# Kernel optimization log

Measured on AMD Instinct MI355X. Metric: run time of the kernel, lower is better.

Reference implementation:

```python
import jax, jax.numpy as jnp
import numpy as np

D = 256        # embedding dim
H = 256        # deriv MLP hidden dim
R = 8          # number of derivation rules
V = 64         # number of thax (axiom) classes
S = 8          # number of sine levels
N_INIT = 8192  # initial clauses
L = 16         # DAG layers
M = 4096       # deriv nodes per layer
N_TOTAL = N_INIT + L * M
POS_WEIGHT_EXTRA = 1.0


def setup_inputs() -> dict:
    key = jax.random.key(0)
    ks = jax.random.split(key, 20)
    inp = {}
    # prob_tweaks (Tweak) is constant-initialized to 0.0 in the original
    inp["prob_tweaks"] = jnp.zeros((4, 2), jnp.float32)
    inp["init_table"] = jax.random.normal(ks[0], (V, D)) * 0.1
    inp["sine_table"] = jax.random.normal(ks[1], (S, D)) * 0.1
    # fan-in scaled so 16 stacked MLP layers stay numerically sane
    inp["W1"] = jax.random.normal(ks[2], (R, 2 * D, H)) / np.float32(np.sqrt(2 * D))
    inp["b1"] = jax.random.normal(ks[3], (R, H)) * 0.01
    inp["t1"] = jax.random.normal(ks[4], (R, H)) * 0.01
    inp["W2"] = jax.random.normal(ks[5], (R, H, D)) / np.float32(np.sqrt(H))
    inp["b2"] = jax.random.normal(ks[6], (R, D)) * 0.01
    inp["w_eval"] = jax.random.normal(ks[7], (D,)) / np.float32(np.sqrt(D))
    inp["b_eval"] = jax.random.normal(ks[8], (1,)) * 0.01
    inp["t_eval"] = jax.random.normal(ks[9], (1,)) * 0.01
    inp["pos"] = jax.random.uniform(ks[10], (N_TOTAL,))
    inp["neg"] = jax.random.uniform(ks[11], (N_TOTAL,))
    inp["init_thax"] = jax.random.randint(ks[12], (N_INIT,), 0, V)
    inp["init_sine"] = jax.random.randint(ks[13], (N_INIT,), 0, S)
    inp["deriv_rule"] = jax.random.randint(ks[14], (L, M), 0, R)
    # parents of layer l must point at already-computed nodes (topological order)
    pk = jax.random.split(ks[15], L)
    pars = [jax.random.randint(pk[l], (M, 2), 0, N_INIT + l * M) for l in range(L)]
    inp["deriv_parents"] = jnp.stack(pars)
    inp["labeled"] = jax.random.randint(ks[16], (N_TOTAL,), 0, 2)
    return inp


def reference(prob_tweaks, init_table, sine_table, W1, b1, t1, W2, b2,
              w_eval, b_eval, t_eval, pos, neg,
              init_thax, init_sine, deriv_rule, deriv_parents, labeled):
    tw_eval = prob_tweaks[0, 0]   # my_tweak[0] for eval_net
    tw_deriv = prob_tweaks[0, 1]  # my_tweak[1] for deriv MLPs

    # init embeddings: per-thax embedding + sine embellishment (USE_SINE)
    emb0 = init_table[init_thax] + sine_table[init_sine]       # [N_INIT, D]
    store = jnp.zeros((N_TOTAL, D), init_table.dtype).at[:N_INIT].set(emb0)

    # layered DAG walk: gather parents, apply rule-specific 2-layer MLP
    for l in range(L):
        x = store[deriv_parents[l]].reshape(M, 2 * D)          # gather parents
        oh = jax.nn.one_hot(deriv_rule[l], R, dtype=x.dtype)   # [M, R] rule dispatch
        h = jax.nn.relu(jnp.einsum('mi,rih->mrh', x, W1)
                        + b1[None] + tw_deriv * t1[None])      # [M, R, H]
        y = jnp.einsum('mrh,rhd->mrd', h, W2) + b2[None]       # [M, R, D]
        emb = jnp.einsum('mrd,mr->md', y, oh)                  # select per-node rule
        store = store.at[N_INIT + l * M:N_INIT + (l + 1) * M].set(emb)

    # eval_net: logit per node with scalar tweak
    vals = store @ w_eval + b_eval[0] + tw_eval * t_eval[0]    # [N_TOTAL]

    lab = labeled.astype(vals.dtype)
    tot = pos + neg
    target = pos / jnp.maximum(tot, 1e-8)
    tot_pos = jnp.sum(pos * lab)
    tot_neg = jnp.sum(neg * lab)
    pw = POS_WEIGHT_EXTRA * tot_neg / jnp.maximum(tot_pos, 1e-8)

    # BCEWithLogitsLoss(pos_weight=pw), contribution weighted by (pos+neg)
    ls = jax.nn.log_sigmoid(vals)
    lns = jax.nn.log_sigmoid(-vals)
    bce = -(pw * target * ls + (1.0 - target) * lns)
    loss = jnp.sum(lab * tot * bce).reshape(1)

    posOK = jnp.sum(lab * pos * (vals >= 0.0))
    negOK = jnp.sum(lab * neg * (vals < 0.0))
    return (loss, posOK, negOK, tot_pos, tot_neg)
```

## Files before the change

kernel.cpp:

```cpp
#include <hip/hip_runtime.h>
#include <math.h>

#define D_    256
#define H_    256
#define R_    8
#define NINIT 8192
#define LL    16
#define MM    4096
#define NTOT  (NINIT + LL*MM)
#define TB    16
#define MP    (MM + R_*TB)
#define NB    (MP/TB)
#define KS1   16
#define KS2   8
#define NT    16
#define EVB   16
#define GE    (NTOT/EVB)

#define EMB_BLKS (NINIT*64/256)
#define PK1_BLKS (R_*KS1*NT*64/256)
#define PK2_BLKS (R_*KS2*NT*64/256)
#define PREP_BLKS (LL + EMB_BLKS + PK1_BLKS + PK2_BLKS)

typedef __attribute__((ext_vector_type(8))) short short8;
typedef __attribute__((ext_vector_type(4))) float f32x4;

__device__ __forceinline__ uint bf16h(float f) {
    uint u = __float_as_uint(f);
    return (u + 0x7fffu + ((u >> 16) & 1u)) >> 16;
}
__device__ __forceinline__ float bf16f(uint h) { return __uint_as_float(h << 16); }

__device__ void sort_body(int l, int t, const int* __restrict__ rule,
                          int* __restrict__ sorted) {
    __shared__ int hist[R_], cursor[R_];
    if (t < R_) hist[t] = 0;
    __syncthreads();
    for (int m = t; m < MM; m += 256) atomicAdd(&hist[rule[l*MM + m]], 1);
    __syncthreads();
    if (t == 0) {
        int off = 0;
        for (int r = 0; r < R_; r++) { cursor[r] = off; off += ((hist[r] + TB - 1)/TB)*TB; }
    }
    for (int m = t; m < MP; m += 256) sorted[l*MP + m] = -1;
    __syncthreads();
    for (int m = t; m < MM; m += 256) {
        int r = rule[l*MM + m];
        int pos = atomicAdd(&cursor[r], 1);
        sorted[l*MP + pos] = m;
    }
}

__device__ void embed_body(int gid, const float* __restrict__ itab,
                           const float* __restrict__ stab,
                           const int* __restrict__ thax, const int* __restrict__ sine,
                           float* __restrict__ store) {
    int n = gid >> 6, d = (gid & 63) << 2;
    int th = thax[n], si = sine[n];
    const float4 a = *(const float4*)&itab[th*D_ + d];
    const float4 b = *(const float4*)&stab[si*D_ + d];
    float4 o; o.x = a.x+b.x; o.y = a.y+b.y; o.z = a.z+b.z; o.w = a.w+b.w;
    *(float4*)&store[(size_t)n*D_ + d] = o;
}

__device__ void pack_body(int gid, const float* __restrict__ W,
                          ushort* __restrict__ Ph, int KSn) {
    int lane = gid & 63;
    int nt   = (gid >> 6) & 15;
    int ks   = (gid >> 10) % KSn;
    int r    = gid / (1024*KSn);
    int K = KSn*32;
    int k0 = ks*32 + (lane >> 4)*8;
    int c  = nt*16 + (lane & 15);
    const float* src = W + ((size_t)r*K + k0)*256 + c;
    uint h[8];
    #pragma unroll
    for (int j = 0; j < 8; j++) h[j] = bf16h(src[(size_t)j*256]);
    size_t o = (size_t)gid*8;
    *(uint4*)&Ph[o] = make_uint4(h[0]|(h[1]<<16), h[2]|(h[3]<<16), h[4]|(h[5]<<16), h[6]|(h[7]<<16));
}

__global__ __launch_bounds__(256) void prep_kernel(
        const int* __restrict__ drule, int* __restrict__ sorted,
        const float* __restrict__ itab, const float* __restrict__ stab,
        const int* __restrict__ thax, const int* __restrict__ sine,
        float* __restrict__ store,
        const float* __restrict__ W1, ushort* __restrict__ P1h,
        const float* __restrict__ W2, ushort* __restrict__ P2h) {
    int b = blockIdx.x, t = threadIdx.x;
    if (b < LL) {
        sort_body(b, t, drule, sorted);
    } else if (b < LL + EMB_BLKS) {
        embed_body((b - LL)*256 + t, itab, stab, thax, sine, store);
    } else if (b < LL + EMB_BLKS + PK1_BLKS) {
        pack_body((b - LL - EMB_BLKS)*256 + t, W1, P1h, KS1);
    } else {
        pack_body((b - LL - EMB_BLKS - PK1_BLKS)*256 + t, W2, P2h, KS2);
    }
}

__global__ __launch_bounds__(1024) void layer_kernel(float* __restrict__ store,
        const int* __restrict__ sorted, const int* __restrict__ rule,
        const int* __restrict__ parents,
        const ushort* __restrict__ P1h, const ushort* __restrict__ P2h,
        const float* __restrict__ b1, const float* __restrict__ t1,
        const float* __restrict__ b2, const float* __restrict__ pt, int l) {
    __shared__ ushort Xh[TB*512], Xl[TB*512];
    __shared__ ushort Hh[TB*256], Hl[TB*256];
    __shared__ int idx_s[TB];
    const int t = threadIdx.x, lane = t & 63, wv = t >> 6;
    if (t < TB) idx_s[t] = sorted[l*MP + blockIdx.x*TB + t];
    __syncthreads();
    if (idx_s[0] < 0) return;
    const int r = rule[l*MM + idx_s[0]];
    const float tw = pt[1];

    {
        const int row = wv;
        const int idx = idx_s[row];
        #pragma unroll
        for (int half = 0; half < 2; half++) {
            float4 v = make_float4(0.f, 0.f, 0.f, 0.f);
            if (idx >= 0) {
                int p = parents[(l*MM + idx)*2 + half];
                v = *(const float4*)&store[(size_t)p*D_ + lane*4];
            }
            uint h0 = bf16h(v.x), h1 = bf16h(v.y), h2 = bf16h(v.z), h3 = bf16h(v.w);
            uint l0 = bf16h(v.x - bf16f(h0)), l1 = bf16h(v.y - bf16f(h1));
            uint l2 = bf16h(v.z - bf16f(h2)), l3 = bf16h(v.w - bf16f(h3));
            int e = half*256 + lane*4;
            int boff = (e*2) ^ ((row & 7) << 4);
            *(uint2*)&Xh[row*512 + (boff >> 1)] = make_uint2(h0|(h1<<16), h2|(h3<<16));
            *(uint2*)&Xl[row*512 + (boff >> 1)] = make_uint2(l0|(l1<<16), l2|(l3<<16));
        }
    }
    __syncthreads();

    const int crow = lane & 15, kg = lane >> 4;
    const int col = wv*16 + crow;

    f32x4 acc;
    { float bb = b1[r*H_ + col] + tw * t1[r*H_ + col]; acc = (f32x4){bb, bb, bb, bb}; }
    const short8* B1hp = (const short8*)P1h + ((size_t)r*KS1*NT + wv)*64 + lane;
    #pragma unroll
    for (int ks = 0; ks < KS1; ks++) {
        int ab = ((ks*64 + kg*16) ^ ((crow & 7) << 4)) >> 1;
        short8 xh = *(const short8*)&Xh[crow*512 + ab];
        short8 xl = *(const short8*)&Xl[crow*512 + ab];
        short8 bh = B1hp[(size_t)ks*NT*64];
        acc = __builtin_amdgcn_mfma_f32_16x16x32_bf16(xl, bh, acc, 0, 0, 0);
        acc = __builtin_amdgcn_mfma_f32_16x16x32_bf16(xh, bh, acc, 0, 0, 0);
    }
    #pragma unroll
    for (int reg = 0; reg < 4; reg++) {
        int row = kg*4 + reg;
        float h = fmaxf(acc[reg], 0.f);
        uint hh = bf16h(h);
        uint hl = bf16h(h - bf16f(hh));
        int boff = (col*2) ^ ((row & 7) << 4);
        Hh[row*256 + (boff >> 1)] = (ushort)hh;
        Hl[row*256 + (boff >> 1)] = (ushort)hl;
    }
    __syncthreads();

    f32x4 acc2;
    { float bb = b2[r*D_ + col]; acc2 = (f32x4){bb, bb, bb, bb}; }
    const short8* B2hp = (const short8*)P2h + ((size_t)r*KS2*NT + wv)*64 + lane;
    #pragma unroll
    for (int ks = 0; ks < KS2; ks++) {
        int ab = ((ks*64 + kg*16) ^ ((crow & 7) << 4)) >> 1;
        short8 hh = *(const short8*)&Hh[crow*256 + ab];
        short8 hl = *(const short8*)&Hl[crow*256 + ab];
        short8 bh = B2hp[(size_t)ks*NT*64];
        acc2 = __builtin_amdgcn_mfma_f32_16x16x32_bf16(hl, bh, acc2, 0, 0, 0);
        acc2 = __builtin_amdgcn_mfma_f32_16x16x32_bf16(hh, bh, acc2, 0, 0, 0);
    }
    const int ob = NINIT + l*MM;
    #pragma unroll
    for (int reg = 0; reg < 4; reg++) {
        int row = kg*4 + reg;
        int idx = idx_s[row];
        if (idx >= 0) store[(size_t)(ob + idx)*D_ + col] = acc2[reg];
    }
}

__global__ __launch_bounds__(256) void eval_kernel(const float* __restrict__ store,
        const float* __restrict__ w_eval, const float* __restrict__ b_eval,
        const float* __restrict__ t_eval, const float* __restrict__ pt,
        const float* __restrict__ pos, const float* __restrict__ neg,
        const int* __restrict__ labeled, float* __restrict__ partials) {
    int t = threadIdx.x, lane = t & 63, wv = t >> 6;
    const float4 w4 = *(const float4*)&w_eval[lane*4];
    const float bev = b_eval[0] + pt[0]*t_eval[0];
    float A = 0.f, B = 0.f, pOK = 0.f, nOK = 0.f, tp = 0.f, tn = 0.f;
    int n0 = blockIdx.x * EVB;
    #pragma unroll
    for (int k = 0; k < 4; k++) {
        int n = n0 + wv*4 + k;
        const float4 s = *(const float4*)&store[(size_t)n*D_ + lane*4];
        float d = s.x*w4.x + s.y*w4.y + s.z*w4.z + s.w*w4.w;
        #pragma unroll
        for (int off = 32; off > 0; off >>= 1) d += __shfl_xor(d, off);
        if (lane == 0) {
            float val = d + bev;
            float lab = (float)labeled[n];
            float p = pos[n], ng = neg[n];
            float tot = p + ng;
            float target = p / fmaxf(tot, 1e-8f);
            float ls  = (val >= 0.f) ? -log1pf(expf(-val)) : (val  - log1pf(expf( val)));
            float lns = (val <= 0.f) ? -log1pf(expf( val)) : (-val - log1pf(expf(-val)));
            A += lab*tot*target*ls;
            B += lab*tot*(1.f - target)*lns;
            if (val >= 0.f) pOK += lab*p; else nOK += lab*ng;
            tp += p*lab; tn += ng*lab;
        }
    }
    __shared__ float red[4][6];
    if (lane == 0) {
        red[wv][0] = A;  red[wv][1] = B;  red[wv][2] = pOK;
        red[wv][3] = nOK; red[wv][4] = tp; red[wv][5] = tn;
    }
    __syncthreads();
    if (t < 6) partials[blockIdx.x*6 + t] = red[0][t] + red[1][t] + red[2][t] + red[3][t];
}

__global__ __launch_bounds__(256) void final_kernel(const float* __restrict__ partials,
                                                    float* __restrict__ out) {
    int t = threadIdx.x;
    float sA=0.f, sB=0.f, sP=0.f, sN=0.f, sTP=0.f, sTN=0.f;
    for (int g = t; g < GE; g += 256) {
        sA  += partials[g*6+0]; sB  += partials[g*6+1]; sP  += partials[g*6+2];
        sN  += partials[g*6+3]; sTP += partials[g*6+4]; sTN += partials[g*6+5];
    }
    __shared__ float red[256];
    #define FRED(V) { __syncthreads(); red[t] = (V); __syncthreads();                     \
        for (int s_ = 128; s_ > 0; s_ >>= 1) { if (t < s_) red[t] += red[t+s_]; __syncthreads(); } \
        (V) = red[0]; __syncthreads(); }
    FRED(sA) FRED(sB) FRED(sP) FRED(sN) FRED(sTP) FRED(sTN)
    #undef FRED
    if (t == 0) {
        float pw = sTN / fmaxf(sTP, 1e-8f);
        out[0] = -(pw*sA + sB);
        out[1] = sP; out[2] = sN; out[3] = sTP; out[4] = sTN;
    }
}

extern "C" void kernel_launch(void* const* d_in, const int* in_sizes, int n_in,
                              void* d_out, int out_size, void* d_ws, size_t ws_size,
                              hipStream_t stream) {
    const float* pt        = (const float*)d_in[0];
    const float* init_tab  = (const float*)d_in[1];
    const float* sine_tab  = (const float*)d_in[2];
    const float* W1        = (const float*)d_in[3];
    const float* b1        = (const float*)d_in[4];
    const float* t1        = (const float*)d_in[5];
    const float* W2        = (const float*)d_in[6];
    const float* b2        = (const float*)d_in[7];
    const float* w_eval    = (const float*)d_in[8];
    const float* b_eval    = (const float*)d_in[9];
    const float* t_eval    = (const float*)d_in[10];
    const float* pos       = (const float*)d_in[11];
    const float* neg       = (const float*)d_in[12];
    const int*   init_thax = (const int*)d_in[13];
    const int*   init_sine = (const int*)d_in[14];
    const int*   drule     = (const int*)d_in[15];
    const int*   dparents  = (const int*)d_in[16];
    const int*   labeled   = (const int*)d_in[17];
    float* out = (float*)d_out;

    char* w = (char*)d_ws;
    const size_t STORE_B = (size_t)NTOT * D_ * 4;
    const size_t SORT_B  = (size_t)LL * MP * 4;
    const size_t P1_B    = (size_t)R_*KS1*NT*64*8*2;
    const size_t P2_B    = (size_t)R_*KS2*NT*64*8*2;
    float*  store    = (float*) w;                    w += STORE_B;
    int*    sorted   = (int*)   w;                    w += SORT_B;
    ushort* P1h      = (ushort*)w;                    w += P1_B;
    ushort* P2h      = (ushort*)w;                    w += P2_B;
    float*  partials = (float*) w;

    prep_kernel<<<PREP_BLKS, 256, 0, stream>>>(drule, sorted, init_tab, sine_tab,
                                               init_thax, init_sine, store,
                                               W1, P1h, W2, P2h);
    for (int l = 0; l < LL; l++)
        layer_kernel<<<NB, 1024, 0, stream>>>(store, sorted, drule, dparents,
                                              P1h, P2h, b1, t1, b2, pt, l);
    eval_kernel <<<GE, 256, 0, stream>>>(store, w_eval, b_eval, t_eval, pt,
                                         pos, neg, labeled, partials);
    final_kernel<<<1,  256, 0, stream>>>(partials, out);
}
```

Measured before the change: 238.2 us.

## Fuse eval logit and BCE partial reductions into embed and layer kernels

The separate eval kernel is removed. Its work now happens where each embedding is produced: init embeddings compute their logit and loss terms in the prep kernel, and each layer block reduces acc2·w_eval across waves and writes per-block loss partials. This avoids re-reading the full 74k×256 fp32 store and saves one launch. The B-weight fragments for both GEMMs are also preloaded into registers before the activation gather, so their global loads overlap with it. The cost is higher register pressure and extra reductions and syncs in the layer kernel.

```diff
diff --git a/kernel.cpp b/kernel.cpp
--- a/kernel.cpp
+++ b/kernel.cpp
@@ -14,13 +14,12 @@
 #define KS1   16
 #define KS2   8
 #define NT    16
-#define EVB   16
-#define GE    (NTOT/EVB)
 
 #define EMB_BLKS (NINIT*64/256)
 #define PK1_BLKS (R_*KS1*NT*64/256)
 #define PK2_BLKS (R_*KS2*NT*64/256)
 #define PREP_BLKS (LL + EMB_BLKS + PK1_BLKS + PK2_BLKS)
+#define NPART (LL*NB + EMB_BLKS)
 
 typedef __attribute__((ext_vector_type(8))) short short8;
 typedef __attribute__((ext_vector_type(4))) float f32x4;
@@ -30,6 +29,20 @@
     return (u + 0x7fffu + ((u >> 16) & 1u)) >> 16;
 }
 __device__ __forceinline__ float bf16f(uint h) { return __uint_as_float(h << 16); }
+
+__device__ __forceinline__ void bce_terms(float val, float lab, float p, float ng,
+                                          float* A, float* B, float* pOK, float* nOK,
+                                          float* tp, float* tn) {
+    float tot = p + ng;
+    float target = p / fmaxf(tot, 1e-8f);
+    float ls  = (val >= 0.f) ? -log1pf(expf(-val)) : (val  - log1pf(expf( val)));
+    float lns = (val <= 0.f) ? -log1pf(expf( val)) : (-val - log1pf(expf(-val)));
+    *A = lab*tot*target*ls;
+    *B = lab*tot*(1.f - target)*lns;
+    *pOK = (val >= 0.f) ? lab*p : 0.f;
+    *nOK = (val <  0.f) ? lab*ng : 0.f;
+    *tp = p*lab; *tn = ng*lab;
+}
 
 __device__ void sort_body(int l, int t, const int* __restrict__ rule,
                           int* __restrict__ sorted) {
@@ -51,16 +64,37 @@
     }
 }
 
-__device__ void embed_body(int gid, const float* __restrict__ itab,
+__device__ void embed_body(int b, int t, const float* __restrict__ itab,
                            const float* __restrict__ stab,
                            const int* __restrict__ thax, const int* __restrict__ sine,
-                           float* __restrict__ store) {
+                           float* __restrict__ store,
+                           const float* __restrict__ w_eval, const float* __restrict__ b_eval,
+                           const float* __restrict__ t_eval, const float* __restrict__ pt,
+                           const float* __restrict__ pos, const float* __restrict__ neg,
+                           const int* __restrict__ labeled, float* __restrict__ partials) {
+    __shared__ float ered[4][6];
+    int gid = b*256 + t;
     int n = gid >> 6, d = (gid & 63) << 2;
     int th = thax[n], si = sine[n];
     const float4 a = *(const float4*)&itab[th*D_ + d];
-    const float4 b = *(const float4*)&stab[si*D_ + d];
-    float4 o; o.x = a.x+b.x; o.y = a.y+b.y; o.z = a.z+b.z; o.w = a.w+b.w;
+    const float4 bb = *(const float4*)&stab[si*D_ + d];
+    float4 o; o.x = a.x+bb.x; o.y = a.y+bb.y; o.z = a.z+bb.z; o.w = a.w+bb.w;
     *(float4*)&store[(size_t)n*D_ + d] = o;
+    const float4 we = *(const float4*)&w_eval[d];
+    float pv = o.x*we.x + o.y*we.y + o.z*we.z + o.w*we.w;
+    #pragma unroll
+    for (int off = 32; off > 0; off >>= 1) pv += __shfl_xor(pv, off);
+    int wvid = t >> 6;
+    if ((t & 63) == 0) {
+        float val = pv + b_eval[0] + pt[0]*t_eval[0];
+        float A, B, pOK, nOK, tp, tn;
+        bce_terms(val, (float)labeled[n], pos[n], neg[n], &A, &B, &pOK, &nOK, &tp, &tn);
+        ered[wvid][0]=A; ered[wvid][1]=B; ered[wvid][2]=pOK;
+        ered[wvid][3]=nOK; ered[wvid][4]=tp; ered[wvid][5]=tn;
+    }
+    __syncthreads();
+    if (t < 6) partials[((size_t)LL*NB + b)*6 + t] =
+        ered[0][t] + ered[1][t] + ered[2][t] + ered[3][t];
 }
 
 __device__ void pack_body(int gid, const float* __restrict__ W,
@@ -86,12 +120,17 @@
         const int* __restrict__ thax, const int* __restrict__ sine,
         float* __restrict__ store,
         const float* __restrict__ W1, ushort* __restrict__ P1h,
-        const float* __restrict__ W2, ushort* __restrict__ P2h) {
+        const float* __restrict__ W2, ushort* __restrict__ P2h,
+        const float* __restrict__ w_eval, const float* __restrict__ b_eval,
+        const float* __restrict__ t_eval, const float* __restrict__ pt,
+        const float* __restrict__ pos, const float* __restrict__ neg,
+        const int* __restrict__ labeled, float* __restrict__ partials) {
     int b = blockIdx.x, t = threadIdx.x;
     if (b < LL) {
         sort_body(b, t, drule, sorted);
     } else if (b < LL + EMB_BLKS) {
-        embed_body((b - LL)*256 + t, itab, stab, thax, sine, store);
+        embed_body(b - LL, t, itab, stab, thax, sine, store,
+                   w_eval, b_eval, t_eval, pt, pos, neg, labeled, partials);
     } else if (b < LL + EMB_BLKS + PK1_BLKS) {
         pack_body((b - LL - EMB_BLKS)*256 + t, W1, P1h, KS1);
     } else {
@@ -104,52 +143,66 @@
         const int* __restrict__ parents,
         const ushort* __restrict__ P1h, const ushort* __restrict__ P2h,
         const float* __restrict__ b1, const float* __restrict__ t1,
-        const float* __restrict__ b2, const float* __restrict__ pt, int l) {
+        const float* __restrict__ b2, const float* __restrict__ pt,
+        const float* __restrict__ w_eval, const float* __restrict__ b_eval,
+        const float* __restrict__ t_eval,
+        const float* __restrict__ pos, const float* __restrict__ neg,
+        const int* __restrict__ labeled, float* __restrict__ partials, int l) {
     __shared__ ushort Xh[TB*512], Xl[TB*512];
     __shared__ ushort Hh[TB*256], Hl[TB*256];
     __shared__ int idx_s[TB];
+    __shared__ float vred[TB][17];
     const int t = threadIdx.x, lane = t & 63, wv = t >> 6;
-    if (t < TB) idx_s[t] = sorted[l*MP + blockIdx.x*TB + t];
-    __syncthreads();
-    if (idx_s[0] < 0) return;
-    const int r = rule[l*MM + idx_s[0]];
-    const float tw = pt[1];
-
-    {
-        const int row = wv;
-        const int idx = idx_s[row];
-        #pragma unroll
-        for (int half = 0; half < 2; half++) {
-            float4 v = make_float4(0.f, 0.f, 0.f, 0.f);
-            if (idx >= 0) {
-                int p = parents[(l*MM + idx)*2 + half];
-                v = *(const float4*)&store[(size_t)p*D_ + lane*4];
-            }
-            uint h0 = bf16h(v.x), h1 = bf16h(v.y), h2 = bf16h(v.z), h3 = bf16h(v.w);
-            uint l0 = bf16h(v.x - bf16f(h0)), l1 = bf16h(v.y - bf16f(h1));
-            uint l2 = bf16h(v.z - bf16f(h2)), l3 = bf16h(v.w - bf16f(h3));
-            int e = half*256 + lane*4;
-            int boff = (e*2) ^ ((row & 7) << 4);
-            *(uint2*)&Xh[row*512 + (boff >> 1)] = make_uint2(h0|(h1<<16), h2|(h3<<16));
-            *(uint2*)&Xl[row*512 + (boff >> 1)] = make_uint2(l0|(l1<<16), l2|(l3<<16));
-        }
-    }
-    __syncthreads();
-
+    const int base = l*MP + blockIdx.x*TB;
+    const int idx0 = sorted[base];
+    if (idx0 < 0) {
+        if (t < 6) partials[((size_t)l*NB + blockIdx.x)*6 + t] = 0.f;
+        return;
+    }
+    const int r = rule[l*MM + idx0];
     const int crow = lane & 15, kg = lane >> 4;
     const int col = wv*16 + crow;
-
-    f32x4 acc;
-    { float bb = b1[r*H_ + col] + tw * t1[r*H_ + col]; acc = (f32x4){bb, bb, bb, bb}; }
+    const float tw = pt[1];
+    const float bev = b_eval[0] + pt[0]*t_eval[0];
+    const float bb1 = b1[r*H_ + col] + tw * t1[r*H_ + col];
+    const float bb2 = b2[r*D_ + col];
+    const float we  = w_eval[col];
+
     const short8* B1hp = (const short8*)P1h + ((size_t)r*KS1*NT + wv)*64 + lane;
+    const short8* B2hp = (const short8*)P2h + ((size_t)r*KS2*NT + wv)*64 + lane;
+    short8 b1r[KS1], b2r[KS2];
+    #pragma unroll
+    for (int ks = 0; ks < KS1; ks++) b1r[ks] = B1hp[(size_t)ks*NT*64];
+    #pragma unroll
+    for (int ks = 0; ks < KS2; ks++) b2r[ks] = B2hp[(size_t)ks*NT*64];
+
+    const int idxr = sorted[base + wv];
+    if (lane == 0) idx_s[wv] = idxr;
+    #pragma unroll
+    for (int half = 0; half < 2; half++) {
+        float4 v = make_float4(0.f, 0.f, 0.f, 0.f);
+        if (idxr >= 0) {
+            int p = parents[(l*MM + idxr)*2 + half];
+            v = *(const float4*)&store[(size_t)p*D_ + lane*4];
+        }
+        uint h0 = bf16h(v.x), h1 = bf16h(v.y), h2 = bf16h(v.z), h3 = bf16h(v.w);
+        uint l0 = bf16h(v.x - bf16f(h0)), l1 = bf16h(v.y - bf16f(h1));
+        uint l2 = bf16h(v.z - bf16f(h2)), l3 = bf16h(v.w - bf16f(h3));
+        int e = half*256 + lane*4;
+        int boff = (e*2) ^ ((wv & 7) << 4);
+        *(uint2*)&Xh[wv*512 + (boff >> 1)] = make_uint2(h0|(h1<<16), h2|(h3<<16));
+        *(uint2*)&Xl[wv*512 + (boff >> 1)] = make_uint2(l0|(l1<<16), l2|(l3<<16));
+    }
+    __syncthreads();
+
+    f32x4 acc = (f32x4){bb1, bb1, bb1, bb1};
     #pragma unroll
     for (int ks = 0; ks < KS1; ks++) {
         int ab = ((ks*64 + kg*16) ^ ((crow & 7) << 4)) >> 1;
         short8 xh = *(const short8*)&Xh[crow*512 + ab];
         short8 xl = *(const short8*)&Xl[crow*512 + ab];
-        short8 bh = B1hp[(size_t)ks*NT*64];
-        acc = __builtin_amdgcn_mfma_f32_16x16x32_bf16(xl, bh, acc, 0, 0, 0);
-        acc = __builtin_amdgcn_mfma_f32_16x16x32_bf16(xh, bh, acc, 0, 0, 0);
+        acc = __builtin_amdgcn_mfma_f32_16x16x32_bf16(xl, b1r[ks], acc, 0, 0, 0);
+        acc = __builtin_amdgcn_mfma_f32_16x16x32_bf16(xh, b1r[ks], acc, 0, 0, 0);
     }
     #pragma unroll
     for (int reg = 0; reg < 4; reg++) {
@@ -163,17 +216,14 @@
     }
     __syncthreads();
 
-    f32x4 acc2;
-    { float bb = b2[r*D_ + col]; acc2 = (f32x4){bb, bb, bb, bb}; }
-    const short8* B2hp = (const short8*)P2h + ((size_t)r*KS2*NT + wv)*64 + lane;
+    f32x4 acc2 = (f32x4){bb2, bb2, bb2, bb2};
     #pragma unroll
     for (int ks = 0; ks < KS2; ks++) {
         int ab = ((ks*64 + kg*16) ^ ((crow & 7) << 4)) >> 1;
         short8 hh = *(const short8*)&Hh[crow*256 + ab];
         short8 hl = *(const short8*)&Hl[crow*256 + ab];
-        short8 bh = B2hp[(size_t)ks*NT*64];
-        acc2 = __builtin_amdgcn_mfma_f32_16x16x32_bf16(hl, bh, acc2, 0, 0, 0);
-        acc2 = __builtin_amdgcn_mfma_f32_16x16x32_bf16(hh, bh, acc2, 0, 0, 0);
+        acc2 = __builtin_amdgcn_mfma_f32_16x16x32_bf16(hl, b2r[ks], acc2, 0, 0, 0);
+        acc2 = __builtin_amdgcn_mfma_f32_16x16x32_bf16(hh, b2r[ks], acc2, 0, 0, 0);
     }
     const int ob = NINIT + l*MM;
     #pragma unroll
@@ -182,53 +232,49 @@
         int idx = idx_s[row];
         if (idx >= 0) store[(size_t)(ob + idx)*D_ + col] = acc2[reg];
     }
-}
-
-__global__ __launch_bounds__(256) void eval_kernel(const float* __restrict__ store,
-        const float* __restrict__ w_eval, const float* __restrict__ b_eval,
-        const float* __restrict__ t_eval, const float* __restrict__ pt,
-        const float* __restrict__ pos, const float* __restrict__ neg,
-        const int* __restrict__ labeled, float* __restrict__ partials) {
-    int t = threadIdx.x, lane = t & 63, wv = t >> 6;
-    const float4 w4 = *(const float4*)&w_eval[lane*4];
-    const float bev = b_eval[0] + pt[0]*t_eval[0];
-    float A = 0.f, B = 0.f, pOK = 0.f, nOK = 0.f, tp = 0.f, tn = 0.f;
-    int n0 = blockIdx.x * EVB;
-    #pragma unroll
-    for (int k = 0; k < 4; k++) {
-        int n = n0 + wv*4 + k;
-        const float4 s = *(const float4*)&store[(size_t)n*D_ + lane*4];
-        float d = s.x*w4.x + s.y*w4.y + s.z*w4.z + s.w*w4.w;
+
+    float pv[4];
+    #pragma unroll
+    for (int reg = 0; reg < 4; reg++) pv[reg] = acc2[reg] * we;
+    #pragma unroll
+    for (int off = 1; off < 16; off <<= 1) {
         #pragma unroll
-        for (int off = 32; off > 0; off >>= 1) d += __shfl_xor(d, off);
-        if (lane == 0) {
-            float val = d + bev;
-            float lab = (float)labeled[n];
-            float p = pos[n], ng = neg[n];
-            float tot = p + ng;
-            float target = p / fmaxf(tot, 1e-8f);
-            float ls  = (val >= 0.f) ? -log1pf(expf(-val)) : (val  - log1pf(expf( val)));
-            float lns = (val <= 0.f) ? -log1pf(expf( val)) : (-val - log1pf(expf(-val)));
-            A += lab*tot*target*ls;
-            B += lab*tot*(1.f - target)*lns;
-            if (val >= 0.f) pOK += lab*p; else nOK += lab*ng;
-            tp += p*lab; tn += ng*lab;
+        for (int reg = 0; reg < 4; reg++) pv[reg] += __shfl_xor(pv[reg], off);
+    }
+    if (crow == 0) {
+        #pragma unroll
+        for (int reg = 0; reg < 4; reg++) vred[kg*4 + reg][wv] = pv[reg];
+    }
+    __syncthreads();
+    if (t < TB) {
+        float val = 0.f;
+        #pragma unroll
+        for (int w16 = 0; w16 < 16; w16++) val += vred[t][w16];
+        int idx = idx_s[t];
+        float A=0.f, B=0.f, pOK=0.f, nOK=0.f, tp=0.f, tn=0.f;
+        if (idx >= 0) {
+            int n = ob + idx;
+            bce_terms(val + bev, (float)labeled[n], pos[n], neg[n],
+                      &A, &B, &pOK, &nOK, &tp, &tn);
         }
-    }
-    __shared__ float red[4][6];
-    if (lane == 0) {
-        red[wv][0] = A;  red[wv][1] = B;  red[wv][2] = pOK;
-        red[wv][3] = nOK; red[wv][4] = tp; red[wv][5] = tn;
-    }
-    __syncthreads();
-    if (t < 6) partials[blockIdx.x*6 + t] = red[0][t] + red[1][t] + red[2][t] + red[3][t];
+        #pragma unroll
+        for (int off = 1; off < 16; off <<= 1) {
+            A   += __shfl_xor(A, off);   B  += __shfl_xor(B, off);
+            pOK += __shfl_xor(pOK, off); nOK += __shfl_xor(nOK, off);
+            tp  += __shfl_xor(tp, off);  tn += __shfl_xor(tn, off);
+        }
+        if (t == 0) {
+            float* ps = &partials[((size_t)l*NB + blockIdx.x)*6];
+            ps[0]=A; ps[1]=B; ps[2]=pOK; ps[3]=nOK; ps[4]=tp; ps[5]=tn;
+        }
+    }
 }
 
 __global__ __launch_bounds__(256) void final_kernel(const float* __restrict__ partials,
                                                     float* __restrict__ out) {
     int t = threadIdx.x;
     float sA=0.f, sB=0.f, sP=0.f, sN=0.f, sTP=0.f, sTN=0.f;
-    for (int g = t; g < GE; g += 256) {
+    for (int g = t; g < NPART; g += 256) {
         sA  += partials[g*6+0]; sB  += partials[g*6+1]; sP  += partials[g*6+2];
         sN  += partials[g*6+3]; sTP += partials[g*6+4]; sTN += partials[g*6+5];
     }
@@ -281,11 +327,13 @@
 
     prep_kernel<<<PREP_BLKS, 256, 0, stream>>>(drule, sorted, init_tab, sine_tab,
                                                init_thax, init_sine, store,
-                                               W1, P1h, W2, P2h);
+                                               W1, P1h, W2, P2h,
+                                               w_eval, b_eval, t_eval, pt,
+                                               pos, neg, labeled, partials);
     for (int l = 0; l < LL; l++)
         layer_kernel<<<NB, 1024, 0, stream>>>(store, sorted, drule, dparents,
-                                              P1h, P2h, b1, t1, b2, pt, l);
-    eval_kernel <<<GE, 256, 0, stream>>>(store, w_eval, b_eval, t_eval, pt,
-                                         pos, neg, labeled, partials);
-    final_kernel<<<1,  256, 0, stream>>>(partials, out);
-}
+                                              P1h, P2h, b1, t1, b2, pt,
+                                              w_eval, b_eval, t_eval,
+                                              pos, neg, labeled, partials, l);
+    final_kernel<<<1, 256, 0, stream>>>(partials, out);
+}
```

Result: slower. 412.2 us (+73.0%).

## Pack rule-sorted nodes densely and loop over rules inside boundary tiles

Applied to the files above, without the earlier changes.

Rows sorted by rule are no longer padded to a tile multiple per rule. Each layer now launches exactly MM/TB tiles, and a tile that straddles a rule boundary runs the MLP once for each rule it contains, storing only the matching rows. This removes padded rows and the launch of up to R partially empty tiles per layer. In exchange it adds extra barriers and repeated MFMA passes on boundary tiles, plus a per-rule loop with a prefix-array lookup. The final reduction is also reworked into an array loop.

```diff
diff --git a/kernel.cpp b/kernel.cpp
--- a/kernel.cpp
+++ b/kernel.cpp
@@ -9,8 +9,7 @@
 #define MM    4096
 #define NTOT  (NINIT + LL*MM)
 #define TB    16
-#define MP    (MM + R_*TB)
-#define NB    (MP/TB)
+#define NTILE (MM/TB)
 #define KS1   16
 #define KS2   8
 #define NT    16
@@ -32,22 +31,22 @@
 __device__ __forceinline__ float bf16f(uint h) { return __uint_as_float(h << 16); }
 
 __device__ void sort_body(int l, int t, const int* __restrict__ rule,
-                          int* __restrict__ sorted) {
-    __shared__ int hist[R_], cursor[R_];
+                          int* __restrict__ sorted, int* __restrict__ prefix) {
+    __shared__ int hist[R_], cursor[R_], pre[R_+1];
     if (t < R_) hist[t] = 0;
     __syncthreads();
     for (int m = t; m < MM; m += 256) atomicAdd(&hist[rule[l*MM + m]], 1);
     __syncthreads();
     if (t == 0) {
-        int off = 0;
-        for (int r = 0; r < R_; r++) { cursor[r] = off; off += ((hist[r] + TB - 1)/TB)*TB; }
-    }
-    for (int m = t; m < MP; m += 256) sorted[l*MP + m] = -1;
-    __syncthreads();
+        pre[0] = 0;
+        for (int r = 0; r < R_; r++) { pre[r+1] = pre[r] + hist[r]; cursor[r] = pre[r]; }
+    }
+    __syncthreads();
+    if (t < R_+1) prefix[l*(R_+1) + t] = pre[t];
     for (int m = t; m < MM; m += 256) {
         int r = rule[l*MM + m];
-        int pos = atomicAdd(&cursor[r], 1);
-        sorted[l*MP + pos] = m;
+        int p = atomicAdd(&cursor[r], 1);
+        sorted[l*MM + p] = m;
     }
 }
 
@@ -81,7 +80,7 @@
 }
 
 __global__ __launch_bounds__(256) void prep_kernel(
-        const int* __restrict__ drule, int* __restrict__ sorted,
+        const int* __restrict__ drule, int* __restrict__ sorted, int* __restrict__ prefix,
         const float* __restrict__ itab, const float* __restrict__ stab,
         const int* __restrict__ thax, const int* __restrict__ sine,
         float* __restrict__ store,
@@ -89,7 +88,7 @@
         const float* __restrict__ W2, ushort* __restrict__ P2h) {
     int b = blockIdx.x, t = threadIdx.x;
     if (b < LL) {
-        sort_body(b, t, drule, sorted);
+        sort_body(b, t, drule, sorted, prefix);
     } else if (b < LL + EMB_BLKS) {
         embed_body((b - LL)*256 + t, itab, stab, thax, sine, store);
     } else if (b < LL + EMB_BLKS + PK1_BLKS) {
@@ -100,7 +99,7 @@
 }
 
 __global__ __launch_bounds__(1024) void layer_kernel(float* __restrict__ store,
-        const int* __restrict__ sorted, const int* __restrict__ rule,
+        const int* __restrict__ sorted, const int* __restrict__ prefix,
         const int* __restrict__ parents,
         const ushort* __restrict__ P1h, const ushort* __restrict__ P2h,
         const float* __restrict__ b1, const float* __restrict__ t1,
@@ -108,79 +107,80 @@
     __shared__ ushort Xh[TB*512], Xl[TB*512];
     __shared__ ushort Hh[TB*256], Hl[TB*256];
     __shared__ int idx_s[TB];
+    __shared__ int pre_s[R_+1];
     const int t = threadIdx.x, lane = t & 63, wv = t >> 6;
-    if (t < TB) idx_s[t] = sorted[l*MP + blockIdx.x*TB + t];
-    __syncthreads();
-    if (idx_s[0] < 0) return;
-    const int r = rule[l*MM + idx_s[0]];
+    if (t < R_+1) pre_s[t] = prefix[l*(R_+1) + t];
     const float tw = pt[1];
 
-    {
-        const int row = wv;
-        const int idx = idx_s[row];
-        #pragma unroll
-        for (int half = 0; half < 2; half++) {
-            float4 v = make_float4(0.f, 0.f, 0.f, 0.f);
-            if (idx >= 0) {
-                int p = parents[(l*MM + idx)*2 + half];
-                v = *(const float4*)&store[(size_t)p*D_ + lane*4];
-            }
-            uint h0 = bf16h(v.x), h1 = bf16h(v.y), h2 = bf16h(v.z), h3 = bf16h(v.w);
-            uint l0 = bf16h(v.x - bf16f(h0)), l1 = bf16h(v.y - bf16f(h1));
-            uint l2 = bf16h(v.z - bf16f(h2)), l3 = bf16h(v.w - bf16f(h3));
-            int e = half*256 + lane*4;
-            int boff = (e*2) ^ ((row & 7) << 4);
-            *(uint2*)&Xh[row*512 + (boff >> 1)] = make_uint2(h0|(h1<<16), h2|(h3<<16));
-            *(uint2*)&Xl[row*512 + (boff >> 1)] = make_uint2(l0|(l1<<16), l2|(l3<<16));
-        }
+    const int m = sorted[l*MM + blockIdx.x*TB + wv];
+    if (lane == 0) idx_s[wv] = m;
+    #pragma unroll
+    for (int half = 0; half < 2; half++) {
+        int p = parents[(l*MM + m)*2 + half];
+        float4 v = *(const float4*)&store[(size_t)p*D_ + lane*4];
+        uint h0 = bf16h(v.x), h1 = bf16h(v.y), h2 = bf16h(v.z), h3 = bf16h(v.w);
+        uint l0 = bf16h(v.x - bf16f(h0)), l1 = bf16h(v.y - bf16f(h1));
+        uint l2 = bf16h(v.z - bf16f(h2)), l3 = bf16h(v.w - bf16f(h3));
+        int e = half*256 + lane*4;
+        int boff = (e*2) ^ ((wv & 7) << 4);
+        *(uint2*)&Xh[wv*512 + (boff >> 1)] = make_uint2(h0|(h1<<16), h2|(h3<<16));
+        *(uint2*)&Xl[wv*512 + (boff >> 1)] = make_uint2(l0|(l1<<16), l2|(l3<<16));
     }
     __syncthreads();
 
     const int crow = lane & 15, kg = lane >> 4;
     const int col = wv*16 + crow;
-
-    f32x4 acc;
-    { float bb = b1[r*H_ + col] + tw * t1[r*H_ + col]; acc = (f32x4){bb, bb, bb, bb}; }
-    const short8* B1hp = (const short8*)P1h + ((size_t)r*KS1*NT + wv)*64 + lane;
-    #pragma unroll
-    for (int ks = 0; ks < KS1; ks++) {
-        int ab = ((ks*64 + kg*16) ^ ((crow & 7) << 4)) >> 1;
-        short8 xh = *(const short8*)&Xh[crow*512 + ab];
-        short8 xl = *(const short8*)&Xl[crow*512 + ab];
-        short8 bh = B1hp[(size_t)ks*NT*64];
-        acc = __builtin_amdgcn_mfma_f32_16x16x32_bf16(xl, bh, acc, 0, 0, 0);
-        acc = __builtin_amdgcn_mfma_f32_16x16x32_bf16(xh, bh, acc, 0, 0, 0);
-    }
-    #pragma unroll
-    for (int reg = 0; reg < 4; reg++) {
-        int row = kg*4 + reg;
-        float h = fmaxf(acc[reg], 0.f);
-        uint hh = bf16h(h);
-        uint hl = bf16h(h - bf16f(hh));
-        int boff = (col*2) ^ ((row & 7) << 4);
-        Hh[row*256 + (boff >> 1)] = (ushort)hh;
-        Hl[row*256 + (boff >> 1)] = (ushort)hl;
-    }
-    __syncthreads();
-
-    f32x4 acc2;
-    { float bb = b2[r*D_ + col]; acc2 = (f32x4){bb, bb, bb, bb}; }
-    const short8* B2hp = (const short8*)P2h + ((size_t)r*KS2*NT + wv)*64 + lane;
-    #pragma unroll
-    for (int ks = 0; ks < KS2; ks++) {
-        int ab = ((ks*64 + kg*16) ^ ((crow & 7) << 4)) >> 1;
-        short8 hh = *(const short8*)&Hh[crow*256 + ab];
-        short8 hl = *(const short8*)&Hl[crow*256 + ab];
-        short8 bh = B2hp[(size_t)ks*NT*64];
-        acc2 = __builtin_amdgcn_mfma_f32_16x16x32_bf16(hl, bh, acc2, 0, 0, 0);
-        acc2 = __builtin_amdgcn_mfma_f32_16x16x32_bf16(hh, bh, acc2, 0, 0, 0);
-    }
+    const int row0 = blockIdx.x*TB;
     const int ob = NINIT + l*MM;
-    #pragma unroll
-    for (int reg = 0; reg < 4; reg++) {
-        int row = kg*4 + reg;
-        int idx = idx_s[row];
-        if (idx >= 0) store[(size_t)(ob + idx)*D_ + col] = acc2[reg];
+
+    for (int r = 0; r < R_; r++) {
+        int lo = (row0 > pre_s[r] ? row0 : pre_s[r]) - row0;
+        int hi = (row0+TB < pre_s[r+1] ? row0+TB : pre_s[r+1]) - row0;
+        if (lo >= hi) continue;
+
+        f32x4 acc;
+        { float bb = b1[r*H_ + col] + tw * t1[r*H_ + col]; acc = (f32x4){bb, bb, bb, bb}; }
+        const short8* B1hp = (const short8*)P1h + ((size_t)r*KS1*NT + wv)*64 + lane;
+        #pragma unroll
+        for (int ks = 0; ks < KS1; ks++) {
+            int ab = ((ks*64 + kg*16) ^ ((crow & 7) << 4)) >> 1;
+            short8 xh = *(const short8*)&Xh[crow*512 + ab];
+            short8 xl = *(const short8*)&Xl[crow*512 + ab];
+            short8 bh = B1hp[(size_t)ks*NT*64];
+            acc = __builtin_amdgcn_mfma_f32_16x16x32_bf16(xl, bh, acc, 0, 0, 0);
+            acc = __builtin_amdgcn_mfma_f32_16x16x32_bf16(xh, bh, acc, 0, 0, 0);
+        }
+        __syncthreads();
+        #pragma unroll
+        for (int reg = 0; reg < 4; reg++) {
+            int row = kg*4 + reg;
+            float h = fmaxf(acc[reg], 0.f);
+            uint hh = bf16h(h);
+            uint hl = bf16h(h - bf16f(hh));
+            int boff = (col*2) ^ ((row & 7) << 4);
+            Hh[row*256 + (boff >> 1)] = (ushort)hh;
+            Hl[row*256 + (boff >> 1)] = (ushort)hl;
+        }
+        __syncthreads();
+
+        f32x4 acc2;
+        { float bb = b2[r*D_ + col]; acc2 = (f32x4){bb, bb, bb, bb}; }
+        const short8* B2hp = (const short8*)P2h + ((size_t)r*KS2*NT + wv)*64 + lane;
+        #pragma unroll
+        for (int ks = 0; ks < KS2; ks++) {
+            int ab = ((ks*64 + kg*16) ^ ((crow & 7) << 4)) >> 1;
+            short8 hh = *(const short8*)&Hh[crow*256 + ab];
+            short8 hl = *(const short8*)&Hl[crow*256 + ab];
+            short8 bh = B2hp[(size_t)ks*NT*64];
+            acc2 = __builtin_amdgcn_mfma_f32_16x16x32_bf16(hl, bh, acc2, 0, 0, 0);
+            acc2 = __builtin_amdgcn_mfma_f32_16x16x32_bf16(hh, bh, acc2, 0, 0, 0);
+        }
+        #pragma unroll
+        for (int reg = 0; reg < 4; reg++) {
+            int row = kg*4 + reg;
+            if (row >= lo && row < hi)
+                store[(size_t)(ob + idx_s[row])*D_ + col] = acc2[reg];
+        }
     }
 }
 
@@ -227,21 +227,27 @@
 __global__ __launch_bounds__(256) void final_kernel(const float* __restrict__ partials,
                                                     float* __restrict__ out) {
     int t = threadIdx.x;
-    float sA=0.f, sB=0.f, sP=0.f, sN=0.f, sTP=0.f, sTN=0.f;
+    float s[6] = {0.f, 0.f, 0.f, 0.f, 0.f, 0.f};
     for (int g = t; g < GE; g += 256) {
-        sA  += partials[g*6+0]; sB  += partials[g*6+1]; sP  += partials[g*6+2];
-        sN  += partials[g*6+3]; sTP += partials[g*6+4]; sTN += partials[g*6+5];
+        #pragma unroll
+        for (int j = 0; j < 6; j++) s[j] += partials[g*6 + j];
     }
     __shared__ float red[256];
-    #define FRED(V) { __syncthreads(); red[t] = (V); __syncthreads();                     \
-        for (int s_ = 128; s_ > 0; s_ >>= 1) { if (t < s_) red[t] += red[t+s_]; __syncthreads(); } \
-        (V) = red[0]; __syncthreads(); }
-    FRED(sA) FRED(sB) FRED(sP) FRED(sN) FRED(sTP) FRED(sTN)
-    #undef FRED
+    #pragma unroll
+    for (int j = 0; j < 6; j++) {
+        __syncthreads();
+        red[t] = s[j];
+        __syncthreads();
+        for (int st = 128; st > 0; st >>= 1) {
+            if (t < st) red[t] += red[t + st];
+            __syncthreads();
+        }
+        s[j] = red[0];
+    }
     if (t == 0) {
-        float pw = sTN / fmaxf(sTP, 1e-8f);
-        out[0] = -(pw*sA + sB);
-        out[1] = sP; out[2] = sN; out[3] = sTP; out[4] = sTN;
+        float pw = s[5] / fmaxf(s[4], 1e-8f);
+        out[0] = -(pw*s[0] + s[1]);
+        out[1] = s[2]; out[2] = s[3]; out[3] = s[4]; out[4] = s[5];
     }
 }
 
@@ -270,22 +276,25 @@
 
     char* w = (char*)d_ws;
     const size_t STORE_B = (size_t)NTOT * D_ * 4;
-    const size_t SORT_B  = (size_t)LL * MP * 4;
+    const size_t SORT_B  = (size_t)LL * MM * 4;
+    const size_t PREF_B  = 1024;
     const size_t P1_B    = (size_t)R_*KS1*NT*64*8*2;
     const size_t P2_B    = (size_t)R_*KS2*NT*64*8*2;
     float*  store    = (float*) w;                    w += STORE_B;
     int*    sorted   = (int*)   w;                    w += SORT_B;
+    int*    prefix   = (int*)   w;                    w += PREF_B;
     ushort* P1h      = (ushort*)w;                    w += P1_B;
     ushort* P2h      = (ushort*)w;                    w += P2_B;
     float*  partials = (float*) w;
 
-    prep_kernel<<<PREP_BLKS, 256, 0, stream>>>(drule, sorted, init_tab, sine_tab,
+    prep_kernel<<<PREP_BLKS, 256, 0, stream>>>(drule, sorted, prefix,
+                                               init_tab, sine_tab,
                                                init_thax, init_sine, store,
                                                W1, P1h, W2, P2h);
     for (int l = 0; l < LL; l++)
-        layer_kernel<<<NB, 1024, 0, stream>>>(store, sorted, drule, dparents,
-                                              P1h, P2h, b1, t1, b2, pt, l);
+        layer_kernel<<<NTILE, 1024, 0, stream>>>(store, sorted, prefix, dparents,
+                                                 P1h, P2h, b1, t1, b2, pt, l);
     eval_kernel <<<GE, 256, 0, stream>>>(store, w_eval, b_eval, t_eval, pt,
                                          pos, neg, labeled, partials);
-    final_kernel<<<1,  256, 0, stream>>>(partials, out);
-}
+    final_kernel<<<1, 256, 0, stream>>>(partials, out);
+}
```

New measurement: 263.3 us. 10.5% more time.
